# Optimization experiments

Measured on AMD Instinct MI355X. Metric: run time of the kernel, lower is better.

Reference implementation:

```python
import math
import jax, jax.numpy as jnp
import numpy as np

N_HEAD = 16
D_MODEL = 1024
D_K = 64
D_V = 64


def setup_inputs() -> dict:
    key = jax.random.key(0)
    ks = jax.random.split(key, 9)
    bs, s = 8, 1024
    q = jax.random.normal(ks[0], (bs, s, D_K), dtype=jnp.float32)
    k = jax.random.normal(ks[1], (bs, s, D_K), dtype=jnp.float32)
    v = jax.random.normal(ks[2], (bs, s, D_V), dtype=jnp.float32)
    # NOTE: the source module only ever uses linear_q (applied to q, k, v alike),
    # so we only materialize that projection. Torch Linear: y = x @ W.T + b.
    Wq = jax.random.normal(ks[3], (N_HEAD * D_K, D_K), dtype=jnp.float32) * 0.02
    bq = jnp.zeros((N_HEAD * D_K,), dtype=jnp.float32)
    W1 = jax.random.normal(ks[4], (D_MODEL, N_HEAD * D_V), dtype=jnp.float32) * 0.02
    b1 = jnp.zeros((D_MODEL,), dtype=jnp.float32)
    W2 = jax.random.normal(ks[5], (D_MODEL, D_MODEL), dtype=jnp.float32) * 0.02
    b2 = jnp.zeros((D_MODEL,), dtype=jnp.float32)
    return {"q": q, "k": k, "v": v, "Wq": Wq, "bq": bq,
            "W1": W1, "b1": b1, "W2": W2, "b2": b2}


def reference(q, k, v, Wq, bq, W1, b1, W2, b2):
    bs, s_q, d_k = q.shape
    h = N_HEAD
    scale = math.sqrt(d_k)
    # shared projection (source uses linear_q for all three); split heads on last dim
    proj = lambda x: (jnp.einsum('bsd,ed->bse', x, Wq) + bq).reshape(bs, -1, h, d_k)
    qh = proj(q)   # [b, s_q, h, d]
    kh = proj(k)   # [b, s_k, h, d]
    vh = proj(v)   # [b, s_v, h, d]
    e = jnp.einsum('bqhd,bkhd->bhqk', qh, kh) / scale
    a = jax.nn.softmax(e, axis=-1)  # dropout = identity in eval mode
    y = jnp.einsum('bhqk,bkhd->bqhd', a, vh).reshape(bs, s_q, h * d_k)
    # output MLP: Linear -> ReLU -> (dropout) -> Linear
    x = jax.nn.relu(jnp.einsum('bsd,ed->bse', y, W1) + b1)
    x = jnp.einsum('bsd,ed->bse', x, W2) + b2
    return x
```

## Files before the change

### kernel.cpp

```cpp
#include <hip/hip_runtime.h>
#include <math.h>

#define NB 8
#define SS 1024
#define NH 16
#define DK 64
#define EE 1024
#define DMOD 1024

using bf16x8 = __attribute__((ext_vector_type(8))) short;
using f32x4  = __attribute__((ext_vector_type(4))) float;

__device__ __forceinline__ unsigned short f2bf(float f) {
    unsigned u = __builtin_bit_cast(unsigned, f);
    u += 0x7FFFu + ((u >> 16) & 1u);
    return (unsigned short)(u >> 16);
}

__device__ __forceinline__ float exp2_hw(float x) {
#if __has_builtin(__builtin_amdgcn_exp2f)
    return __builtin_amdgcn_exp2f(x);
#else
    float r; asm("v_exp_f32 %0, %1" : "=v"(r) : "v"(x)); return r;
#endif
}

__device__ __forceinline__ unsigned cvt_pk_bf16(float lo, float hi) {
    unsigned r;
    asm("v_cvt_pk_bf16_f32 %0, %1, %2" : "=v"(r) : "v"(lo), "v"(hi));
    return r;
}

__device__ __forceinline__ void gld16(const void* g, void* l) {
    __builtin_amdgcn_global_load_lds(
        (const __attribute__((address_space(1))) void*)g,
        (__attribute__((address_space(3))) void*)l, 16, 0, 0);
}

__global__ __launch_bounds__(256) void cvt_all(
    const float* __restrict__ W1, const float* __restrict__ W2,
    const float* __restrict__ q, const float* __restrict__ k,
    const float* __restrict__ v, const float* __restrict__ Wq,
    unsigned short* __restrict__ W1b, unsigned short* __restrict__ W2b,
    unsigned short* __restrict__ qb, unsigned short* __restrict__ kb,
    unsigned short* __restrict__ vb, unsigned short* __restrict__ Wqb)
{
    const int z = blockIdx.y;
    const float* s; unsigned short* d; int n;
    switch (z) {
        case 0:  s = W1; d = W1b; n = 1048576; break;
        case 1:  s = W2; d = W2b; n = 1048576; break;
        case 2:  s = q;  d = qb;  n = 524288;  break;
        case 3:  s = k;  d = kb;  n = 524288;  break;
        case 4:  s = v;  d = vb;  n = 524288;  break;
        default: s = Wq; d = Wqb; n = 65536;   break;
    }
    const int i = (blockIdx.x * 256 + threadIdx.x) * 8;
    if (i >= n) return;
    const float4 a = *(const float4*)(s + i);
    const float4 b = *(const float4*)(s + i + 4);
    bf16x8 o;
    o[0]=(short)f2bf(a.x); o[1]=(short)f2bf(a.y); o[2]=(short)f2bf(a.z); o[3]=(short)f2bf(a.w);
    o[4]=(short)f2bf(b.x); o[5]=(short)f2bf(b.y); o[6]=(short)f2bf(b.z); o[7]=(short)f2bf(b.w);
    *(bf16x8*)(d + i) = o;
}

__global__ __launch_bounds__(256) void proj_mfma(
    const unsigned short* __restrict__ qb, const unsigned short* __restrict__ kb,
    const unsigned short* __restrict__ vb, const unsigned short* __restrict__ Wb,
    const float* __restrict__ bias, unsigned short* __restrict__ Cbase,
    float qscale)
{
    __shared__ __align__(16) unsigned short As[128 * 64];
    __shared__ __align__(16) unsigned short Bs[128 * 64];
    const int z = blockIdx.z;
    const unsigned short* X = (z == 0) ? qb : (z == 1) ? kb : vb;
    unsigned short* C = Cbase + (size_t)z * 8388608;
    const float sc = (z == 0) ? qscale : 1.0f;
    const int tid  = threadIdx.x;
    const int lane = tid & 63;
    const int w = tid >> 6, wm = w >> 1, wn = w & 1;
    const int n0 = blockIdx.x * 128, m0 = blockIdx.y * 128;
    const int lr = lane & 15, lg = lane >> 4;

    #pragma unroll
    for (int p = 0; p < 4; ++p) {
        const int c = p * 256 + tid;
        const int lb = (p * 256 + (tid & ~63)) * 8;
        gld16(X  + (size_t)m0 * DK + (size_t)c * 8, As + lb);
        gld16(Wb + (size_t)n0 * DK + (size_t)c * 8, Bs + lb);
    }
    __syncthreads();

    f32x4 acc[4][4] = {};
    #pragma unroll
    for (int kk = 0; kk < 2; ++kk) {
        bf16x8 af[4], bfr[4];
        #pragma unroll
        for (int mf = 0; mf < 4; ++mf)
            af[mf] = *(const bf16x8*)&As[(wm * 64 + mf * 16 + lr) * 64 + kk * 32 + lg * 8];
        #pragma unroll
        for (int nf = 0; nf < 4; ++nf)
            bfr[nf] = *(const bf16x8*)&Bs[(wn * 64 + nf * 16 + lr) * 64 + kk * 32 + lg * 8];
        #pragma unroll
        for (int mf = 0; mf < 4; ++mf)
            #pragma unroll
            for (int nf = 0; nf < 4; ++nf)
                acc[mf][nf] = __builtin_amdgcn_mfma_f32_16x16x32_bf16(
                    af[mf], bfr[nf], acc[mf][nf], 0, 0, 0);
    }

    #pragma unroll
    for (int nf = 0; nf < 4; ++nf) {
        const int n = n0 + wn * 64 + nf * 16 + lr;
        const float bb = bias[n];
        #pragma unroll
        for (int mf = 0; mf < 4; ++mf)
            #pragma unroll
            for (int r = 0; r < 4; ++r) {
                const int mr = m0 + wm * 64 + mf * 16 + lg * 4 + r;
                const int bh = (mr >> 10) * NH + (n >> 6);
                const int s  = mr & 1023, d = n & 63;
                const size_t idx = (z == 2)
                    ? (size_t)bh * 65536 + (size_t)d * 1024 + s
                    : (size_t)bh * 65536 + (size_t)s * 64 + d;
                C[idx] = f2bf((acc[mf][nf][r] + bb) * sc);
            }
    }
}

__global__ __launch_bounds__(256) void attn_v8(
    const unsigned short* __restrict__ Qp, const unsigned short* __restrict__ Kp,
    const unsigned short* __restrict__ Vt, unsigned short* __restrict__ Y)
{
    __shared__ __align__(16) unsigned short Ks[64 * 64];
    __shared__ __align__(16) unsigned short Vs[64 * 64];
    __shared__ __align__(16) unsigned short Ps[4][16][72];
    const int tid  = threadIdx.x;
    const int lane = tid & 63;
    const int w    = tid >> 6;
    const int flat    = blockIdx.x;
    const int logical = (flat & 7) * 256 + (flat >> 3);
    const int qt = logical & 15;
    const int bh = logical >> 4;
    const int q0 = qt * 64;
    const size_t base = (size_t)bh * (SS * DK);
    const int lr = lane & 15, lg = lane >> 4;
    const int lg4 = lg * 4;

    const int c0 = tid,       r0 = c0 >> 3, h0 = c0 & 7;
    const int c1 = 256 + tid, r1 = c1 >> 3, h1 = c1 & 7;
    const int lds0 = r0 * 64 + ((h0 ^ (r0 & 7)) << 3);
    const int lds1 = r1 * 64 + ((h1 ^ (r1 & 7)) << 3);

    const unsigned short* kbase = Kp + base;
    const unsigned short* vbase = Vt + base;
    bf16x8 kA = *(const bf16x8*)(kbase + (size_t)r0 * DK + h0 * 8);
    bf16x8 kB = *(const bf16x8*)(kbase + (size_t)r1 * DK + h1 * 8);
    bf16x8 vA = *(const bf16x8*)(vbase + (size_t)r0 * SS + h0 * 8);
    bf16x8 vB = *(const bf16x8*)(vbase + (size_t)r1 * SS + h1 * 8);
    *(bf16x8*)&Ks[lds0] = kA; *(bf16x8*)&Ks[lds1] = kB;
    *(bf16x8*)&Vs[lds0] = vA; *(bf16x8*)&Vs[lds1] = vB;

    const unsigned short* qptr = Qp + base + (size_t)(q0 + w * 16 + lr) * DK + lg * 8;
    const bf16x8 bQ0 = *(const bf16x8*)qptr;
    const bf16x8 bQ1 = *(const bf16x8*)(qptr + 32);

    __syncthreads();

    float m = -1e30f, l = 0.0f;
    f32x4 oacc[4] = {};

    for (int kt = 0; kt < 16; ++kt) {
        if (kt < 15) {
            const int s1 = (kt + 1) * 64;
            kA = *(const bf16x8*)(kbase + (size_t)(s1 + r0) * DK + h0 * 8);
            kB = *(const bf16x8*)(kbase + (size_t)(s1 + r1) * DK + h1 * 8);
            vA = *(const bf16x8*)(vbase + (size_t)r0 * SS + s1 + h0 * 8);
            vB = *(const bf16x8*)(vbase + (size_t)r1 * SS + s1 + h1 * 8);
        }

        f32x4 sacc[4];
        #pragma unroll
        for (int nb = 0; nb < 4; ++nb) {
            const int krow = nb * 16 + lr;
            const bf16x8 aK0 = *(const bf16x8*)&Ks[krow * 64 + ((lg       ^ (lr & 7)) << 3)];
            const bf16x8 aK1 = *(const bf16x8*)&Ks[krow * 64 + (((4 + lg) ^ (lr & 7)) << 3)];
            f32x4 z = {};
            z = __builtin_amdgcn_mfma_f32_16x16x32_bf16(aK0, bQ0, z, 0, 0, 0);
            z = __builtin_amdgcn_mfma_f32_16x16x32_bf16(aK1, bQ1, z, 0, 0, 0);
            sacc[nb] = z;
        }

        bf16x8 bV[2][4];
        #pragma unroll
        for (int kk = 0; kk < 2; ++kk)
            #pragma unroll
            for (int d0 = 0; d0 < 4; ++d0) {
                const int vrow = d0 * 16 + lr;
                bV[kk][d0] = *(const bf16x8*)&Vs[vrow * 64 + (((kk * 4 + lg) ^ (lr & 7)) << 3)];
            }

        float mx = sacc[0][0];
        #pragma unroll
        for (int nb = 0; nb < 4; ++nb)
            #pragma unroll
            for (int r = 0; r < 4; ++r)
                mx = fmaxf(mx, sacc[nb][r]);
        mx = fmaxf(mx, __shfl_xor(mx, 16));
        mx = fmaxf(mx, __shfl_xor(mx, 32));

        if (__any(mx > m + 8.0f)) {
            const float mn = fmaxf(m, mx);
            const float alpha = exp2_hw(m - mn);
            m = mn;
            l *= alpha;
            #pragma unroll
            for (int r = 0; r < 4; ++r) {
                const float ar = __shfl(alpha, lg4 + r, 16);
                #pragma unroll
                for (int d0 = 0; d0 < 4; ++d0) oacc[d0][r] *= ar;
            }
        }

        float p[4][4];
        float ls = 0.0f;
        #pragma unroll
        for (int nb = 0; nb < 4; ++nb)
            #pragma unroll
            for (int r = 0; r < 4; ++r) {
                const float pv = exp2_hw(sacc[nb][r] - m);
                p[nb][r] = pv;
                ls += pv;
            }
        ls += __shfl_xor(ls, 16);
        ls += __shfl_xor(ls, 32);
        l += ls;

        #pragma unroll
        for (int nb = 0; nb < 4; ++nb) {
            uint2 pw;
            pw.x = cvt_pk_bf16(p[nb][0], p[nb][1]);
            pw.y = cvt_pk_bf16(p[nb][2], p[nb][3]);
            *(uint2*)&Ps[w][lr][nb * 16 + lg4] = pw;
        }

        #pragma unroll
        for (int kk = 0; kk < 2; ++kk) {
            const bf16x8 aP = *(const bf16x8*)&Ps[w][lr][kk * 32 + lg * 8];
            #pragma unroll
            for (int d0 = 0; d0 < 4; ++d0)
                oacc[d0] = __builtin_amdgcn_mfma_f32_16x16x32_bf16(aP, bV[kk][d0], oacc[d0], 0, 0, 0);
        }

        if (kt < 15) {
            __syncthreads();
            *(bf16x8*)&Ks[lds0] = kA; *(bf16x8*)&Ks[lds1] = kB;
            *(bf16x8*)&Vs[lds0] = vA; *(bf16x8*)&Vs[lds1] = vB;
            __syncthreads();
        }
    }

    const float linv = 1.0f / l;
    const int hh = bh & 15, bb = bh >> 4;
    #pragma unroll
    for (int r = 0; r < 4; ++r) {
        const float lri = __shfl(linv, lg4 + r, 16);
        const int qr = q0 + w * 16 + lg4 + r;
        unsigned short* dst = Y + (size_t)(bb * SS + qr) * EE + hh * DK;
        #pragma unroll
        for (int d0 = 0; d0 < 4; ++d0)
            dst[d0 * 16 + lr] = f2bf(oacc[d0][r] * lri);
    }
}

template<bool RELU, bool OUT_BF16>
__global__ __launch_bounds__(256) void mlp_gemm(
    const unsigned short* __restrict__ A, const unsigned short* __restrict__ B,
    const float* __restrict__ bias, void* __restrict__ Cv)
{
    constexpr int K = 1024, N = 1024;
    __shared__ __align__(16) unsigned short As[128 * 64];
    __shared__ __align__(16) unsigned short Bs[128 * 64];
    const int tid  = threadIdx.x;
    const int lane = tid & 63;
    const int w = tid >> 6, wm = w >> 1, wn = w & 1;
    const int flat    = blockIdx.x;
    const int logical = (flat & 7) * 64 + (flat >> 3);
    const int n0 = (logical & 7) * 128, m0 = (logical >> 3) * 128;
    const int lr = lane & 15, lg = lane >> 4;

    f32x4 acc[4][4] = {};

    for (int kt = 0; kt < K; kt += 64) {
        __syncthreads();
        #pragma unroll
        for (int p = 0; p < 4; ++p) {
            const int c = p * 256 + tid;
            const int row = c >> 3, col = (c & 7) * 8;
            const int lb = (p * 256 + (tid & ~63)) * 8;
            gld16(A + (size_t)(m0 + row) * K + kt + col, As + lb);
            gld16(B + (size_t)(n0 + row) * K + kt + col, Bs + lb);
        }
        __syncthreads();
        #pragma unroll
        for (int kk = 0; kk < 2; ++kk) {
            bf16x8 af[4], bfr[4];
            #pragma unroll
            for (int mf = 0; mf < 4; ++mf)
                af[mf] = *(const bf16x8*)&As[(wm * 64 + mf * 16 + lr) * 64 + kk * 32 + lg * 8];
            #pragma unroll
            for (int nf = 0; nf < 4; ++nf)
                bfr[nf] = *(const bf16x8*)&Bs[(wn * 64 + nf * 16 + lr) * 64 + kk * 32 + lg * 8];
            #pragma unroll
            for (int mf = 0; mf < 4; ++mf)
                #pragma unroll
                for (int nf = 0; nf < 4; ++nf)
                    acc[mf][nf] = __builtin_amdgcn_mfma_f32_16x16x32_bf16(
                        af[mf], bfr[nf], acc[mf][nf], 0, 0, 0);
        }
    }

    #pragma unroll
    for (int nf = 0; nf < 4; ++nf) {
        const int cc = n0 + wn * 64 + nf * 16 + lr;
        const float bb = bias[cc];
        #pragma unroll
        for (int mf = 0; mf < 4; ++mf) {
            #pragma unroll
            for (int r = 0; r < 4; ++r) {
                float x = acc[mf][nf][r] + bb;
                if (RELU) x = fmaxf(x, 0.0f);
                const size_t rr = (size_t)(m0 + wm * 64 + mf * 16 + lg * 4 + r);
                if (OUT_BF16) ((unsigned short*)Cv)[rr * N + cc] = f2bf(x);
                else          ((float*)Cv)[rr * N + cc] = x;
            }
        }
    }
}

extern "C" void kernel_launch(void* const* d_in, const int* in_sizes, int n_in,
                              void* d_out, int out_size, void* d_ws, size_t ws_size,
                              hipStream_t stream) {
    const float* q  = (const float*)d_in[0];
    const float* k  = (const float*)d_in[1];
    const float* v  = (const float*)d_in[2];
    const float* Wq = (const float*)d_in[3];
    const float* bq = (const float*)d_in[4];
    const float* W1 = (const float*)d_in[5];
    const float* b1 = (const float*)d_in[6];
    const float* W2 = (const float*)d_in[7];
    const float* b2 = (const float*)d_in[8];

    unsigned short* wsu = (unsigned short*)d_ws;
    unsigned short* Qp  = wsu;
    unsigned short* Kp  = wsu + (size_t)8388608;
    unsigned short* Vt  = wsu + (size_t)16777216;
    unsigned short* Y   = wsu + (size_t)25165824;
    unsigned short* W1b = wsu + (size_t)33554432;
    unsigned short* W2b = wsu + (size_t)34603008;
    unsigned short* qb  = wsu + (size_t)35651584;
    unsigned short* kb  = wsu + (size_t)36175872;
    unsigned short* vb  = wsu + (size_t)36700160;
    unsigned short* Wqb = wsu + (size_t)37224448;
    unsigned short* H1  = Qp;

    dim3 blk(256);

    cvt_all<<<dim3(512, 6), blk, 0, stream>>>(W1, W2, q, k, v, Wq,
                                              W1b, W2b, qb, kb, vb, Wqb);

    const float qscale = 0.125f * 1.44269504088896340736f;
    proj_mfma<<<dim3(8, 64, 3), blk, 0, stream>>>(qb, kb, vb, Wqb, bq, Qp, qscale);

    attn_v8<<<2048, blk, 0, stream>>>(Qp, Kp, Vt, Y);

    mlp_gemm<true,  true ><<<512, blk, 0, stream>>>(Y,  W1b, b1, H1);
    mlp_gemm<false, false><<<512, blk, 0, stream>>>(H1, W2b, b2, d_out);
}
```

Baseline: 158.2 us.

## Double attention query tile per block to reuse K/V tiles across two query fragments

Each wave now handles two 16-row query fragments (128 queries per block instead of 64), so every K/V tile loaded into shared memory feeds twice as many MFMAs. This halves the grid and halves total K/V global loads and LDS fills per query. In exchange it raises register pressure (two sets of accumulators, scores and softmax state), which may cut occupancy, and leaves fewer blocks to spread across CUs.

```diff
diff --git a/kernel.cpp b/kernel.cpp
--- a/kernel.cpp
+++ b/kernel.cpp
@@ -129,21 +129,21 @@
     }
 }
 
-__global__ __launch_bounds__(256) void attn_v8(
+__global__ __launch_bounds__(256) void attn_v9(
     const unsigned short* __restrict__ Qp, const unsigned short* __restrict__ Kp,
     const unsigned short* __restrict__ Vt, unsigned short* __restrict__ Y)
 {
     __shared__ __align__(16) unsigned short Ks[64 * 64];
     __shared__ __align__(16) unsigned short Vs[64 * 64];
-    __shared__ __align__(16) unsigned short Ps[4][16][72];
+    __shared__ __align__(16) unsigned short Ps[4][32][72];
     const int tid  = threadIdx.x;
     const int lane = tid & 63;
     const int w    = tid >> 6;
     const int flat    = blockIdx.x;
-    const int logical = (flat & 7) * 256 + (flat >> 3);
-    const int qt = logical & 15;
-    const int bh = logical >> 4;
-    const int q0 = qt * 64;
+    const int logical = (flat & 7) * 128 + (flat >> 3);
+    const int qt = logical & 7;
+    const int bh = logical >> 3;
+    const int q0 = qt * 128;
     const size_t base = (size_t)bh * (SS * DK);
     const int lr = lane & 15, lg = lane >> 4;
     const int lg4 = lg * 4;
@@ -162,14 +162,19 @@
     *(bf16x8*)&Ks[lds0] = kA; *(bf16x8*)&Ks[lds1] = kB;
     *(bf16x8*)&Vs[lds0] = vA; *(bf16x8*)&Vs[lds1] = vB;
 
-    const unsigned short* qptr = Qp + base + (size_t)(q0 + w * 16 + lr) * DK + lg * 8;
-    const bf16x8 bQ0 = *(const bf16x8*)qptr;
-    const bf16x8 bQ1 = *(const bf16x8*)(qptr + 32);
+    bf16x8 bQ[2][2];
+    #pragma unroll
+    for (int qf = 0; qf < 2; ++qf) {
+        const unsigned short* qptr =
+            Qp + base + (size_t)(q0 + w * 32 + qf * 16 + lr) * DK + lg * 8;
+        bQ[qf][0] = *(const bf16x8*)qptr;
+        bQ[qf][1] = *(const bf16x8*)(qptr + 32);
+    }
 
     __syncthreads();
 
-    float m = -1e30f, l = 0.0f;
-    f32x4 oacc[4] = {};
+    float m[2] = {-1e30f, -1e30f}, l[2] = {0.0f, 0.0f};
+    f32x4 oacc[2][4] = {};
 
     for (int kt = 0; kt < 16; ++kt) {
         if (kt < 15) {
@@ -180,16 +185,19 @@
             vB = *(const bf16x8*)(vbase + (size_t)r1 * SS + s1 + h1 * 8);
         }
 
-        f32x4 sacc[4];
+        f32x4 sacc[2][4];
         #pragma unroll
         for (int nb = 0; nb < 4; ++nb) {
             const int krow = nb * 16 + lr;
             const bf16x8 aK0 = *(const bf16x8*)&Ks[krow * 64 + ((lg       ^ (lr & 7)) << 3)];
             const bf16x8 aK1 = *(const bf16x8*)&Ks[krow * 64 + (((4 + lg) ^ (lr & 7)) << 3)];
-            f32x4 z = {};
-            z = __builtin_amdgcn_mfma_f32_16x16x32_bf16(aK0, bQ0, z, 0, 0, 0);
-            z = __builtin_amdgcn_mfma_f32_16x16x32_bf16(aK1, bQ1, z, 0, 0, 0);
-            sacc[nb] = z;
+            #pragma unroll
+            for (int qf = 0; qf < 2; ++qf) {
+                f32x4 z = {};
+                z = __builtin_amdgcn_mfma_f32_16x16x32_bf16(aK0, bQ[qf][0], z, 0, 0, 0);
+                z = __builtin_amdgcn_mfma_f32_16x16x32_bf16(aK1, bQ[qf][1], z, 0, 0, 0);
+                sacc[qf][nb] = z;
+            }
         }
 
         bf16x8 bV[2][4];
@@ -201,56 +209,60 @@
                 bV[kk][d0] = *(const bf16x8*)&Vs[vrow * 64 + (((kk * 4 + lg) ^ (lr & 7)) << 3)];
             }
 
-        float mx = sacc[0][0];
-        #pragma unroll
-        for (int nb = 0; nb < 4; ++nb)
-            #pragma unroll
-            for (int r = 0; r < 4; ++r)
-                mx = fmaxf(mx, sacc[nb][r]);
-        mx = fmaxf(mx, __shfl_xor(mx, 16));
-        mx = fmaxf(mx, __shfl_xor(mx, 32));
-
-        if (__any(mx > m + 8.0f)) {
-            const float mn = fmaxf(m, mx);
-            const float alpha = exp2_hw(m - mn);
-            m = mn;
-            l *= alpha;
-            #pragma unroll
-            for (int r = 0; r < 4; ++r) {
-                const float ar = __shfl(alpha, lg4 + r, 16);
-                #pragma unroll
-                for (int d0 = 0; d0 < 4; ++d0) oacc[d0][r] *= ar;
-            }
-        }
-
-        float p[4][4];
-        float ls = 0.0f;
-        #pragma unroll
-        for (int nb = 0; nb < 4; ++nb)
-            #pragma unroll
-            for (int r = 0; r < 4; ++r) {
-                const float pv = exp2_hw(sacc[nb][r] - m);
-                p[nb][r] = pv;
-                ls += pv;
-            }
-        ls += __shfl_xor(ls, 16);
-        ls += __shfl_xor(ls, 32);
-        l += ls;
-
-        #pragma unroll
-        for (int nb = 0; nb < 4; ++nb) {
-            uint2 pw;
-            pw.x = cvt_pk_bf16(p[nb][0], p[nb][1]);
-            pw.y = cvt_pk_bf16(p[nb][2], p[nb][3]);
-            *(uint2*)&Ps[w][lr][nb * 16 + lg4] = pw;
-        }
-
-        #pragma unroll
-        for (int kk = 0; kk < 2; ++kk) {
-            const bf16x8 aP = *(const bf16x8*)&Ps[w][lr][kk * 32 + lg * 8];
-            #pragma unroll
-            for (int d0 = 0; d0 < 4; ++d0)
-                oacc[d0] = __builtin_amdgcn_mfma_f32_16x16x32_bf16(aP, bV[kk][d0], oacc[d0], 0, 0, 0);
+        #pragma unroll
+        for (int qf = 0; qf < 2; ++qf) {
+            float mx = sacc[qf][0][0];
+            #pragma unroll
+            for (int nb = 0; nb < 4; ++nb)
+                #pragma unroll
+                for (int r = 0; r < 4; ++r)
+                    mx = fmaxf(mx, sacc[qf][nb][r]);
+            mx = fmaxf(mx, __shfl_xor(mx, 16));
+            mx = fmaxf(mx, __shfl_xor(mx, 32));
+
+            if (__any(mx > m[qf] + 8.0f)) {
+                const float mn = fmaxf(m[qf], mx);
+                const float alpha = exp2_hw(m[qf] - mn);
+                m[qf] = mn;
+                l[qf] *= alpha;
+                #pragma unroll
+                for (int r = 0; r < 4; ++r) {
+                    const float ar = __shfl(alpha, lg4 + r, 16);
+                    #pragma unroll
+                    for (int d0 = 0; d0 < 4; ++d0) oacc[qf][d0][r] *= ar;
+                }
+            }
+
+            float p[4][4];
+            float ls = 0.0f;
+            #pragma unroll
+            for (int nb = 0; nb < 4; ++nb)
+                #pragma unroll
+                for (int r = 0; r < 4; ++r) {
+                    const float pv = exp2_hw(sacc[qf][nb][r] - m[qf]);
+                    p[nb][r] = pv;
+                    ls += pv;
+                }
+            ls += __shfl_xor(ls, 16);
+            ls += __shfl_xor(ls, 32);
+            l[qf] += ls;
+
+            #pragma unroll
+            for (int nb = 0; nb < 4; ++nb) {
+                uint2 pw;
+                pw.x = cvt_pk_bf16(p[nb][0], p[nb][1]);
+                pw.y = cvt_pk_bf16(p[nb][2], p[nb][3]);
+                *(uint2*)&Ps[w][qf * 16 + lr][nb * 16 + lg4] = pw;
+            }
+
+            #pragma unroll
+            for (int kk = 0; kk < 2; ++kk) {
+                const bf16x8 aP = *(const bf16x8*)&Ps[w][qf * 16 + lr][kk * 32 + lg * 8];
+                #pragma unroll
+                for (int d0 = 0; d0 < 4; ++d0)
+                    oacc[qf][d0] = __builtin_amdgcn_mfma_f32_16x16x32_bf16(
+                        aP, bV[kk][d0], oacc[qf][d0], 0, 0, 0);
+            }
         }
 
         if (kt < 15) {
@@ -261,16 +273,19 @@
         }
     }
 
-    const float linv = 1.0f / l;
     const int hh = bh & 15, bb = bh >> 4;
     #pragma unroll
-    for (int r = 0; r < 4; ++r) {
-        const float lri = __shfl(linv, lg4 + r, 16);
-        const int qr = q0 + w * 16 + lg4 + r;
-        unsigned short* dst = Y + (size_t)(bb * SS + qr) * EE + hh * DK;
-        #pragma unroll
-        for (int d0 = 0; d0 < 4; ++d0)
-            dst[d0 * 16 + lr] = f2bf(oacc[d0][r] * lri);
+    for (int qf = 0; qf < 2; ++qf) {
+        const float linv = 1.0f / l[qf];
+        #pragma unroll
+        for (int r = 0; r < 4; ++r) {
+            const float lri = __shfl(linv, lg4 + r, 16);
+            const int qr = q0 + w * 32 + qf * 16 + lg4 + r;
+            unsigned short* dst = Y + (size_t)(bb * SS + qr) * EE + hh * DK;
+            #pragma unroll
+            for (int d0 = 0; d0 < 4; ++d0)
+                dst[d0 * 16 + lr] = f2bf(oacc[qf][d0][r] * lri);
+        }
     }
 }
 
@@ -373,7 +388,7 @@
     const float qscale = 0.125f * 1.44269504088896340736f;
     proj_mfma<<<dim3(8, 64, 3), blk, 0, stream>>>(qb, kb, vb, Wqb, bq, Qp, qscale);
 
-    attn_v8<<<2048, blk, 0, stream>>>(Qp, Kp, Vt, Y);
+    attn_v9<<<1024, blk, 0, stream>>>(Qp, Kp, Vt, Y);
 
     mlp_gemm<true,  true ><<<512, blk, 0, stream>>>(Y,  W1b, b1, H1);
     mlp_gemm<false, false><<<512, blk, 0, stream>>>(H1, W2b, b2, d_out);
```

Result: faster. 152.8 us (-3.4%).
